# Kernel tuning notes

Hardware: AMD Instinct MI355X
Metric: run time of the kernel (lower is better)

Reference implementation:

```python
import jax, jax.numpy as jnp
import numpy as np

B, L = 32, 512
H, W = 352, 1216
MAXLEN = max(H, W)  # max Bresenham path length after clipping to image


def setup_inputs() -> dict:
    key = jax.random.key(0)
    k1, k2 = jax.random.split(key)
    pred = jax.random.normal(k1, (B, 1, H, W), dtype=jnp.float32)
    lines = jax.random.randint(k2, (B, L, 2, 2), 0, 1216, dtype=jnp.int32)
    return {"pred": pred, "lines": lines}


def _bresenham_paths(lines):
    # lines: [B, L, 2, 2] int32, last dim = (x, y), coords already clipped.
    # Closed-form skimage/Bresenham: along the major axis i=0..dmaj,
    # minor_i = min0 + smin * floor((2*dmin*i + dmaj) / (2*dmaj)).
    x0 = lines[..., 0, 0]; y0 = lines[..., 0, 1]
    x1 = lines[..., 1, 0]; y1 = lines[..., 1, 1]
    dx = jnp.abs(x1 - x0); dy = jnp.abs(y1 - y0)
    xmajor = dx > dy  # skimage 'steep' swap: x is major iff |dx| > |dy|
    dmaj = jnp.where(xmajor, dx, dy)
    dmin = jnp.where(xmajor, dy, dx)
    smaj = jnp.where(xmajor, jnp.sign(x1 - x0), jnp.sign(y1 - y0))
    smin = jnp.where(xmajor, jnp.sign(y1 - y0), jnp.sign(x1 - x0))
    maj0 = jnp.where(xmajor, x0, y0)
    min0 = jnp.where(xmajor, y0, x0)
    i = jnp.arange(MAXLEN, dtype=jnp.int32)
    # Clamp step index to dmaj -> padding repeats the endpoint, so diffs there are 0.
    i_eff = jnp.minimum(i[None, None, :], dmaj[..., None])       # [B, L, MAXLEN]
    dmaj_e = dmaj[..., None]
    dmaj_safe = jnp.maximum(dmaj_e, 1)
    maj = maj0[..., None] + smaj[..., None] * i_eff
    minr = min0[..., None] + smin[..., None] * (
        (2 * dmin[..., None] * i_eff + dmaj_e) // (2 * dmaj_safe))
    xs = jnp.where(xmajor[..., None], maj, minr)
    ys = jnp.where(xmajor[..., None], minr, maj)
    return xs, ys


def reference(pred, lines):
    # Clip coords into the image, exactly like the torch module.
    x = jnp.clip(lines[..., 0], 0, W - 1)
    y = jnp.clip(lines[..., 1], 0, H - 1)
    lines_c = jnp.stack([x, y], axis=-1)                          # [B, L, 2, 2]

    xs, ys = _bresenham_paths(lines_c)                            # [B, L, MAXLEN]
    p = pred.reshape(B, H * W)
    idx = (ys * W + xs).reshape(B, -1)
    vals = jnp.take_along_axis(p, idx, axis=1).reshape(B, L, MAXLEN)

    # Sum of |diff| of depth along each line (padding repeats endpoint -> 0 diff).
    diff_sums = jnp.sum(jnp.abs(jnp.diff(vals, axis=-1)), axis=-1)  # [B, L]
    # Skip lines whose endpoint depth gap < 0.5 (data-dependent skip -> mask).
    end_diff = jnp.abs(vals[..., 0] - vals[..., -1])
    diff_sums = jnp.where(end_diff < 0.5, 0.0, diff_sums)

    # Angle-based weights (computed from clipped lines, as in the original).
    lf = lines_c.astype(jnp.float32)
    slopes = jnp.abs((lf[:, :, 1, 1] - lf[:, :, 0, 1]) /
                     (lf[:, :, 1, 0] - lf[:, :, 0, 0] + 1e-6))
    degrees = (jnp.arctan(slopes) * 180.0 / jnp.pi) % 90.0
    mx = jnp.max(degrees, axis=1, keepdims=True)                  # per-sample max
    skew_factor = 1.5
    skewed = degrees ** skew_factor / (mx + 1.0) ** (skew_factor - 1.0)
    sharp = 2.5
    heights = 90.0 - (jnp.abs(skewed - 45.0) ** sharp) ** (1.0 / sharp)
    weights = (heights / 300.0) ** 4

    return jnp.sum(weights * diff_sums)
```

## Files before the change

### kernel.cpp

```cpp
#include <hip/hip_runtime.h>
#include <math.h>

#define BB 32
#define LL 512
#define HH 352
#define WW 1216
#define NLINES (BB * LL)
#define WAVES_PER_BLOCK 4
#define NBLOCKS (NLINES / WAVES_PER_BLOCK)

typedef float f4 __attribute__((ext_vector_type(4), aligned(4)));

__device__ __forceinline__ float line_degree(int x0, int y0, int x1, int y1) {
    float slope = fabsf(((float)y1 - (float)y0) / ((float)x1 - (float)x0 + 1e-6f));
    float deg = (atanf(slope) * 180.0f) / 3.14159274101257324f;
    return fmodf(deg, 90.0f);
}

__global__ void __launch_bounds__(256) line_walk_kernel(
        const float* __restrict__ pred, const int* __restrict__ lines,
        float* __restrict__ partials) {
    int lane = threadIdx.x & 63;
    int w = threadIdx.x >> 6;
    int bid = blockIdx.x;
    int swz = (bid & 7) * (NBLOCKS / 8) + (bid >> 3);
    int g = swz * WAVES_PER_BLOCK + w;
    int b = g >> 9;

    int4 ln = ((const int4*)lines)[g];
    int x0 = min(max(ln.x, 0), WW - 1);
    int y0 = min(max(ln.y, 0), HH - 1);
    int x1 = min(max(ln.z, 0), WW - 1);
    int y1 = min(max(ln.w, 0), HH - 1);

    int dx = abs(x1 - x0), dy = abs(y1 - y0);
    bool xm = dx > dy;
    int dmaj = xm ? dx : dy;
    int dmin = xm ? dy : dx;

    const float* __restrict__ p = pred + (size_t)b * (HH * WW);

    float vf = p[y0 * WW + x0];
    float vl = p[y1 * WW + x1];
    bool active = (fabsf(vf - vl) >= 0.5f) && (dmaj > 0);

    float s = 0.0f;
    if (active) {
        if (dy == 0) {
            int rb = y0 * WW;
            int xlo = min(x0, x1);
            int dxs = dmaj;
            int PV = dxs & ~3;
            int nch = (PV + 255) >> 8;
            for (int j = 0; j < nch; ++j) {
                int p0 = (j << 8) + (lane << 2);
                bool act = p0 < PV;
                int c = rb + xlo + (act ? p0 : 0);
                f4 lo = *(const f4*)(p + c);
                f4 hi = *(const f4*)(p + c + 1);
                if (act) {
                    s += fabsf(hi.x - lo.x) + fabsf(hi.y - lo.y)
                       + fabsf(hi.z - lo.z) + fabsf(hi.w - lo.w);
                }
            }
            if (lane < 3) {
                int i = PV + lane;
                if (i < dxs) {
                    float a  = p[rb + xlo + i];
                    float bv = p[rb + xlo + i + 1];
                    s += fabsf(bv - a);
                }
            }
        } else {
            int sx = (x1 > x0) - (x1 < x0);
            int sy = (y1 > y0) - (y1 < y0);
            int smaj = xm ? sx : sy;
            int smin = xm ? sy : sx;
            int maj0 = xm ? x0 : y0;
            int min0 = xm ? y0 : x0;
            unsigned den = 2u * (unsigned)dmaj;
            int tdm = 2 * dmin;
            unsigned M = 0xFFFFFFFFu / den + 1u;
            int sA = xm ? 1 : WW;
            int sB = xm ? WW : 1;
            int A = smaj * sA;
            int Bm = smin * sB;
            int off0 = maj0 * sA + min0 * sB;
            int niter = (dmaj + 62) / 63;
            int nbatch = (niter + 7) >> 3;
            int idx = lane;
            for (int t = 0; t < nbatch; ++t, idx += 504) {
                int offs[8];
                #pragma unroll
                for (int k = 0; k < 8; ++k) {
                    int idc = min(idx + 63 * k, dmaj);
                    unsigned num = (unsigned)(tdm * idc) + (unsigned)dmaj;
                    unsigned q = __umulhi(num, M);
                    q -= (q * den > num) ? 1u : 0u;
                    offs[k] = off0 + idc * A + (int)q * Bm;
                }
                float v[8];
                #pragma unroll
                for (int k = 0; k < 8; ++k) v[k] = p[offs[k]];
                #pragma unroll
                for (int k = 0; k < 8; ++k) {
                    float vn = __shfl_down(v[k], 1);
                    float d = fabsf(vn - v[k]);
                    s += (lane < 63) ? d : 0.0f;
                }
            }
        }
        #pragma unroll
        for (int offr = 32; offr > 0; offr >>= 1) s += __shfl_down(s, offr);
    }

    if (lane == 0) {
        partials[g] = active ? s : 0.0f;
    }
}

__global__ void finalize_kernel(const int* __restrict__ lines,
                                const float* __restrict__ partials,
                                float* __restrict__ out) {
    __shared__ float red[LL];
    int b = blockIdx.x;
    int t = threadIdx.x;
    int g = b * LL + t;
    int4 ln = ((const int4*)lines)[g];
    int x0 = min(max(ln.x, 0), WW - 1);
    int y0 = min(max(ln.y, 0), HH - 1);
    int x1 = min(max(ln.z, 0), WW - 1);
    int y1 = min(max(ln.w, 0), HH - 1);
    float deg = line_degree(x0, y0, x1, y1);
    red[t] = deg;
    __syncthreads();
    for (int s = LL / 2; s > 0; s >>= 1) {
        if (t < s) red[t] = fmaxf(red[t], red[t + s]);
        __syncthreads();
    }
    float mxv = red[0];
    __syncthreads();
    float skewed = (deg * sqrtf(deg)) / sqrtf(mxv + 1.0f);
    float tt = fabsf(skewed - 45.0f);
    float h = 90.0f - tt;
    float hw = h * (1.0f / 300.0f);
    float hw2 = hw * hw;
    float wgt = hw2 * hw2;
    red[t] = wgt * partials[g];
    __syncthreads();
    for (int s = LL / 2; s > 0; s >>= 1) {
        if (t < s) red[t] += red[t + s];
        __syncthreads();
    }
    if (t == 0) atomicAdd(out, red[0]);
}

extern "C" void kernel_launch(void* const* d_in, const int* in_sizes, int n_in,
                              void* d_out, int out_size, void* d_ws, size_t ws_size,
                              hipStream_t stream) {
    const float* pred = (const float*)d_in[0];
    const int* lines = (const int*)d_in[1];
    float* out = (float*)d_out;
    float* partials = (float*)d_ws;

    hipMemsetAsync(out, 0, sizeof(float), stream);
    line_walk_kernel<<<NBLOCKS, 256, 0, stream>>>(pred, lines, partials);
    finalize_kernel<<<BB, LL, 0, stream>>>(lines, partials, out);
}
```

Before: 24.91 us.

## Process two lines per wave and replace memset+atomic with counter-based final reduction

Each wavefront now walks two lines instead of one, halving the block count and letting endpoint loads for both lines be issued together to overlap latency. The hipMemsetAsync launch is removed: the walk kernel resets a counter, and the finalize kernel writes per-sample sums and has the last block to finish sum them deterministically into the output. This cuts one launch and the float atomic, but pairs lines serially in a wave, which may worsen load imbalance between long and short lines.

```diff
diff --git a/kernel.cpp b/kernel.cpp
--- a/kernel.cpp
+++ b/kernel.cpp
@@ -6,8 +6,8 @@
 #define HH 352
 #define WW 1216
 #define NLINES (BB * LL)
-#define WAVES_PER_BLOCK 4
-#define NBLOCKS (NLINES / WAVES_PER_BLOCK)
+#define LPW 2
+#define NBLK2 (NLINES / (LPW * 4))
 
 typedef float f4 __attribute__((ext_vector_type(4), aligned(4)));
 
@@ -17,110 +17,130 @@
     return fmodf(deg, 90.0f);
 }
 
+__device__ __forceinline__ float walk_line(const float* __restrict__ p, int lane,
+        int x0, int y0, int x1, int y1, int dy, bool xm, int dmaj, int dmin) {
+    float s = 0.0f;
+    if (dy == 0) {
+        int rb = y0 * WW;
+        int xlo = min(x0, x1);
+        int dxs = dmaj;
+        int PV = dxs & ~3;
+        int nch = (PV + 255) >> 8;
+        for (int j = 0; j < nch; ++j) {
+            int p0 = (j << 8) + (lane << 2);
+            bool act = p0 < PV;
+            int c = rb + xlo + (act ? p0 : 0);
+            f4 lo = *(const f4*)(p + c);
+            f4 hi = *(const f4*)(p + c + 1);
+            if (act) {
+                s += fabsf(hi.x - lo.x) + fabsf(hi.y - lo.y)
+                   + fabsf(hi.z - lo.z) + fabsf(hi.w - lo.w);
+            }
+        }
+        if (lane < 3) {
+            int i = PV + lane;
+            if (i < dxs) {
+                float a  = p[rb + xlo + i];
+                float bv = p[rb + xlo + i + 1];
+                s += fabsf(bv - a);
+            }
+        }
+    } else {
+        int sx = (x1 > x0) - (x1 < x0);
+        int sy = (y1 > y0) - (y1 < y0);
+        int smaj = xm ? sx : sy;
+        int smin = xm ? sy : sx;
+        int maj0 = xm ? x0 : y0;
+        int min0 = xm ? y0 : x0;
+        unsigned den = 2u * (unsigned)dmaj;
+        int tdm = 2 * dmin;
+        unsigned M = 0xFFFFFFFFu / den + 1u;
+        int sA = xm ? 1 : WW;
+        int sB = xm ? WW : 1;
+        int A = smaj * sA;
+        int Bm = smin * sB;
+        int off0 = maj0 * sA + min0 * sB;
+        int niter = (dmaj + 62) / 63;
+        int nbatch = (niter + 7) >> 3;
+        int idx = lane;
+        for (int t = 0; t < nbatch; ++t, idx += 504) {
+            int offs[8];
+            #pragma unroll
+            for (int k = 0; k < 8; ++k) {
+                int idc = min(idx + 63 * k, dmaj);
+                unsigned num = (unsigned)(tdm * idc) + (unsigned)dmaj;
+                unsigned q = __umulhi(num, M);
+                q -= (q * den > num) ? 1u : 0u;
+                offs[k] = off0 + idc * A + (int)q * Bm;
+            }
+            float v[8];
+            #pragma unroll
+            for (int k = 0; k < 8; ++k) v[k] = p[offs[k]];
+            #pragma unroll
+            for (int k = 0; k < 8; ++k) {
+                float vn = __shfl_down(v[k], 1);
+                float d = fabsf(vn - v[k]);
+                s += (lane < 63) ? d : 0.0f;
+            }
+        }
+    }
+    return s;
+}
+
 __global__ void __launch_bounds__(256) line_walk_kernel(
         const float* __restrict__ pred, const int* __restrict__ lines,
-        float* __restrict__ partials) {
+        float* __restrict__ partials, unsigned* __restrict__ counter) {
+    if (blockIdx.x == 0 && threadIdx.x == 0) *counter = 0;
     int lane = threadIdx.x & 63;
     int w = threadIdx.x >> 6;
     int bid = blockIdx.x;
-    int swz = (bid & 7) * (NBLOCKS / 8) + (bid >> 3);
-    int g = swz * WAVES_PER_BLOCK + w;
-    int b = g >> 9;
-
-    int4 ln = ((const int4*)lines)[g];
-    int x0 = min(max(ln.x, 0), WW - 1);
-    int y0 = min(max(ln.y, 0), HH - 1);
-    int x1 = min(max(ln.z, 0), WW - 1);
-    int y1 = min(max(ln.w, 0), HH - 1);
-
-    int dx = abs(x1 - x0), dy = abs(y1 - y0);
-    bool xm = dx > dy;
-    int dmaj = xm ? dx : dy;
-    int dmin = xm ? dy : dx;
+    int swz = (bid & 7) * (NBLK2 / 8) + (bid >> 3);
+    int W = swz * 4 + w;
+    int g0 = W * LPW, g1 = g0 + 1;
+    int b = g0 >> 9;
+
+    int4 lA = ((const int4*)lines)[g0];
+    int4 lB = ((const int4*)lines)[g1];
+    int ax0 = min(max(lA.x, 0), WW - 1), ay0 = min(max(lA.y, 0), HH - 1);
+    int ax1 = min(max(lA.z, 0), WW - 1), ay1 = min(max(lA.w, 0), HH - 1);
+    int bx0 = min(max(lB.x, 0), WW - 1), by0 = min(max(lB.y, 0), HH - 1);
+    int bx1 = min(max(lB.z, 0), WW - 1), by1 = min(max(lB.w, 0), HH - 1);
 
     const float* __restrict__ p = pred + (size_t)b * (HH * WW);
 
-    float vf = p[y0 * WW + x0];
-    float vl = p[y1 * WW + x1];
-    bool active = (fabsf(vf - vl) >= 0.5f) && (dmaj > 0);
-
-    float s = 0.0f;
-    if (active) {
-        if (dy == 0) {
-            int rb = y0 * WW;
-            int xlo = min(x0, x1);
-            int dxs = dmaj;
-            int PV = dxs & ~3;
-            int nch = (PV + 255) >> 8;
-            for (int j = 0; j < nch; ++j) {
-                int p0 = (j << 8) + (lane << 2);
-                bool act = p0 < PV;
-                int c = rb + xlo + (act ? p0 : 0);
-                f4 lo = *(const f4*)(p + c);
-                f4 hi = *(const f4*)(p + c + 1);
-                if (act) {
-                    s += fabsf(hi.x - lo.x) + fabsf(hi.y - lo.y)
-                       + fabsf(hi.z - lo.z) + fabsf(hi.w - lo.w);
-                }
-            }
-            if (lane < 3) {
-                int i = PV + lane;
-                if (i < dxs) {
-                    float a  = p[rb + xlo + i];
-                    float bv = p[rb + xlo + i + 1];
-                    s += fabsf(bv - a);
-                }
-            }
-        } else {
-            int sx = (x1 > x0) - (x1 < x0);
-            int sy = (y1 > y0) - (y1 < y0);
-            int smaj = xm ? sx : sy;
-            int smin = xm ? sy : sx;
-            int maj0 = xm ? x0 : y0;
-            int min0 = xm ? y0 : x0;
-            unsigned den = 2u * (unsigned)dmaj;
-            int tdm = 2 * dmin;
-            unsigned M = 0xFFFFFFFFu / den + 1u;
-            int sA = xm ? 1 : WW;
-            int sB = xm ? WW : 1;
-            int A = smaj * sA;
-            int Bm = smin * sB;
-            int off0 = maj0 * sA + min0 * sB;
-            int niter = (dmaj + 62) / 63;
-            int nbatch = (niter + 7) >> 3;
-            int idx = lane;
-            for (int t = 0; t < nbatch; ++t, idx += 504) {
-                int offs[8];
-                #pragma unroll
-                for (int k = 0; k < 8; ++k) {
-                    int idc = min(idx + 63 * k, dmaj);
-                    unsigned num = (unsigned)(tdm * idc) + (unsigned)dmaj;
-                    unsigned q = __umulhi(num, M);
-                    q -= (q * den > num) ? 1u : 0u;
-                    offs[k] = off0 + idc * A + (int)q * Bm;
-                }
-                float v[8];
-                #pragma unroll
-                for (int k = 0; k < 8; ++k) v[k] = p[offs[k]];
-                #pragma unroll
-                for (int k = 0; k < 8; ++k) {
-                    float vn = __shfl_down(v[k], 1);
-                    float d = fabsf(vn - v[k]);
-                    s += (lane < 63) ? d : 0.0f;
-                }
-            }
-        }
-        #pragma unroll
-        for (int offr = 32; offr > 0; offr >>= 1) s += __shfl_down(s, offr);
-    }
-
+    float vfA = p[ay0 * WW + ax0];
+    float vlA = p[ay1 * WW + ax1];
+    float vfB = p[by0 * WW + bx0];
+    float vlB = p[by1 * WW + bx1];
+
+    int adx = abs(ax1 - ax0), ady = abs(ay1 - ay0);
+    bool axm = adx > ady;
+    int admaj = axm ? adx : ady, admin_ = axm ? ady : adx;
+    int bdx = abs(bx1 - bx0), bdy = abs(by1 - by0);
+    bool bxm = bdx > bdy;
+    int bdmaj = bxm ? bdx : bdy, bdmin = bxm ? bdy : bdx;
+
+    bool actA = (fabsf(vfA - vlA) >= 0.5f) && (admaj > 0);
+    bool actB = (fabsf(vfB - vlB) >= 0.5f) && (bdmaj > 0);
+
+    float s0 = actA ? walk_line(p, lane, ax0, ay0, ax1, ay1, ady, axm, admaj, admin_) : 0.0f;
+    float s1 = actB ? walk_line(p, lane, bx0, by0, bx1, by1, bdy, bxm, bdmaj, bdmin) : 0.0f;
+
+    #pragma unroll
+    for (int off = 32; off > 0; off >>= 1) {
+        s0 += __shfl_down(s0, off);
+        s1 += __shfl_down(s1, off);
+    }
     if (lane == 0) {
-        partials[g] = active ? s : 0.0f;
+        partials[g0] = actA ? s0 : 0.0f;
+        partials[g1] = actB ? s1 : 0.0f;
     }
 }
 
 __global__ void finalize_kernel(const int* __restrict__ lines,
                                 const float* __restrict__ partials,
+                                float* __restrict__ bsum,
+                                unsigned* __restrict__ counter,
                                 float* __restrict__ out) {
     __shared__ float red[LL];
     int b = blockIdx.x;
@@ -152,7 +172,17 @@
         if (t < s) red[t] += red[t + s];
         __syncthreads();
     }
-    if (t == 0) atomicAdd(out, red[0]);
+    if (t == 0) {
+        bsum[b] = red[0];
+        __threadfence();
+        if (atomicAdd(counter, 1u) == BB - 1) {
+            __threadfence();
+            float tot = 0.0f;
+            #pragma unroll
+            for (int i = 0; i < BB; ++i) tot += bsum[i];
+            out[0] = tot;
+        }
+    }
 }
 
 extern "C" void kernel_launch(void* const* d_in, const int* in_sizes, int n_in,
@@ -161,9 +191,11 @@
     const float* pred = (const float*)d_in[0];
     const int* lines = (const int*)d_in[1];
     float* out = (float*)d_out;
-    float* partials = (float*)d_ws;
-
-    hipMemsetAsync(out, 0, sizeof(float), stream);
-    line_walk_kernel<<<NBLOCKS, 256, 0, stream>>>(pred, lines, partials);
-    finalize_kernel<<<BB, LL, 0, stream>>>(lines, partials, out);
-}
+    float* ws = (float*)d_ws;
+    float* partials = ws;
+    float* bsum = ws + NLINES;
+    unsigned* counter = (unsigned*)(ws + NLINES + BB);
+
+    line_walk_kernel<<<NBLK2, 256, 0, stream>>>(pred, lines, partials, counter);
+    finalize_kernel<<<BB, LL, 0, stream>>>(lines, partials, bsum, counter, out);
+}
```

Measured after the change: 21.66 us. 13.1% less time.
